# Kernel tuning notes

Hardware: AMD Instinct MI355X
Metric: run time of the kernel (lower is better)

The kernel has to match this reference:

```python
import jax, jax.numpy as jnp
import numpy as np

BLOCK = 32      # block_size
KB = 128        # K // BLOCK (mask rows)
NB = 128        # N // BLOCK (mask cols)
DENSITY = 0.1


def _make_mask_indices():
    rng = np.random.RandomState(0)
    mask = rng.rand(KB, NB) < DENSITY
    # guarantee no fully-empty output column (kernel writes zeros there anyway,
    # segment_sum also yields zeros, so this is only to keep stats sane)
    ii, jj = np.nonzero(mask)   # row-major order == torch.nonzero(mask)
    return ii.astype(np.int32), jj.astype(np.int32)


def setup_inputs() -> dict:
    key = jax.random.key(0)
    k1, k2 = jax.random.split(key)
    ii, jj = _make_mask_indices()
    nnz = ii.shape[0]
    M = 4096
    K = KB * BLOCK
    x = jax.random.normal(k1, (M, K), dtype=jnp.float32)
    # block-sparse weight: one [BLOCK, BLOCK] tile per nonzero mask entry,
    # stored in row-major nonzero order (matches torch.nonzero ordering)
    w = jax.random.normal(k2, (nnz, BLOCK, BLOCK), dtype=jnp.float32) * 0.02
    return {"x": x, "w": w, "idx_i": jnp.asarray(ii), "idx_j": jnp.asarray(jj)}


def reference(x, w, idx_i, idx_j):
    # y[:, j*B:(j+1)*B] += x[:, i*B:(i+1)*B] @ w[blk] for each nonzero block (i, j)
    M, K = x.shape
    nnz, B, _ = w.shape
    xb = x.reshape(M, K // B, B)[:, idx_i, :]                 # [M, nnz, B] gather
    partial = jnp.einsum('mnk,nkj->nmj', xb, w)               # [nnz, M, B]
    yb = jax.ops.segment_sum(partial, idx_j, num_segments=NB)  # [NB, M, B] scatter-add
    return yb.transpose(1, 0, 2).reshape(M, NB * B)           # [M, N]
```

## Files before the change

kernel.cpp:

```cpp
#include <hip/hip_runtime.h>
#include <hip/hip_bf16.h>

typedef __bf16 bf16x8 __attribute__((ext_vector_type(8)));
typedef __bf16 bf16x4 __attribute__((ext_vector_type(4)));
typedef float f32x4 __attribute__((ext_vector_type(4)));

#define KDIM 4096
#define NDIM 4096
#define NBJ  128
#define KB   128

#define NB      7
#define BLK_LDS 2560

__global__ __launch_bounds__(256) void k_prep(
    const float* __restrict__ x, const float* __restrict__ w,
    const int* __restrict__ idx_i, const int* __restrict__ idx_j,
    __bf16* __restrict__ xb, __bf16* __restrict__ wT,
    int* __restrict__ colptr, int* __restrict__ colinfo,
    int nnz, int M, int nbCvt) {
    __shared__ char smem[2176];
    int b = blockIdx.x, t = threadIdx.x;

    if (b < nbCvt) {
        int i  = b & (KB - 1);
        int m0 = (b >> 7) * 64;
        int q  = t & 3, r = t >> 2;
        const float* xp = x + (size_t)(m0 + r) * KDIM + i * 32 + q * 8;
        float4 u = ((const float4*)xp)[0];
        float4 v = ((const float4*)xp)[1];
        bf16x8 o;
        o[0]=(__bf16)u.x; o[1]=(__bf16)u.y; o[2]=(__bf16)u.z; o[3]=(__bf16)u.w;
        o[4]=(__bf16)v.x; o[5]=(__bf16)v.y; o[6]=(__bf16)v.z; o[7]=(__bf16)v.w;
        *(bf16x8*)(xb + ((size_t)i * M + m0 + r) * 32 + q * 8) = o;
    } else if (b < nbCvt + nnz) {
        auto tile = (__bf16(*)[33])smem;
        int n = b - nbCvt;
        float4 v = ((const float4*)(w + (size_t)n * 1024))[t];
        int e = t * 4, k = e >> 5, c = e & 31;
        tile[k][c + 0] = (__bf16)v.x; tile[k][c + 1] = (__bf16)v.y;
        tile[k][c + 2] = (__bf16)v.z; tile[k][c + 3] = (__bf16)v.w;
        __syncthreads();
        int f = t * 4, cc = f >> 5, kk = f & 31;
        bf16x4 o;
        o[0] = tile[kk + 0][cc]; o[1] = tile[kk + 1][cc];
        o[2] = tile[kk + 2][cc]; o[3] = tile[kk + 3][cc];
        ((bf16x4*)(wT + (size_t)n * 1024))[t] = o;
    } else {
        int* cnt = (int*)smem;
        int* cur = cnt + NBJ;
        if (t < NBJ) cnt[t] = 0;
        __syncthreads();
        for (int n = t; n < nnz; n += 256) atomicAdd(&cnt[idx_j[n]], 1);
        __syncthreads();
        int mycount = (t < NBJ) ? cnt[t] : 0;
        for (int off = 1; off < NBJ; off <<= 1) {
            int add = (t < NBJ && t >= off) ? cnt[t - off] : 0;
            __syncthreads();
            if (t < NBJ) cnt[t] += add;
            __syncthreads();
        }
        if (t < NBJ) {
            colptr[t + 1] = cnt[t];
            cur[t] = cnt[t] - mycount;
            if (t == 0) colptr[0] = 0;
        }
        __syncthreads();
        for (int n = t; n < nnz; n += 256) {
            int j = idx_j[n];
            int pos = atomicAdd(&cur[j], 1);
            colinfo[pos] = (idx_i[n] << 16) | n;
        }
    }
}

struct AFrag { bf16x8 a0, a1; };

#define MFMA4(A, B0, B1)                                                       \
    acc[0][0] = __builtin_amdgcn_mfma_f32_16x16x32_bf16(A.a0, B0, acc[0][0], 0, 0, 0); \
    acc[0][1] = __builtin_amdgcn_mfma_f32_16x16x32_bf16(A.a0, B1, acc[0][1], 0, 0, 0); \
    acc[1][0] = __builtin_amdgcn_mfma_f32_16x16x32_bf16(A.a1, B0, acc[1][0], 0, 0, 0); \
    acc[1][1] = __builtin_amdgcn_mfma_f32_16x16x32_bf16(A.a1, B1, acc[1][1], 0, 0, 0);

__global__ __launch_bounds__(256, 8) void k_bsmm(
    const __bf16* __restrict__ xb, const __bf16* __restrict__ wT,
    const int* __restrict__ colptr, const int* __restrict__ colinfo,
    float* __restrict__ y, int M) {
    __shared__ int nfo[NB];
    __shared__ __attribute__((aligned(16))) char wbuf[NB * BLK_LDS];

    int RCH = M >> 7;
    int l = blockIdx.x;
    int rc, j;
    if ((RCH & 7) == 0) {
        int rps = RCH >> 3;
        int s = l & 7, u = l >> 3;
        rc = s * rps + (u >> 7);
        j  = u & (NBJ - 1);
    } else {
        rc = l % RCH; j = l / RCH;
    }
    int t = threadIdx.x;
    int lane = t & 63, wave = t >> 6;
    int quad = lane >> 4, l16 = lane & 15;
    int wrow = rc * 128 + wave * 32;

    int beg = colptr[j], end = colptr[j + 1];

    f32x4 acc[2][2] = {};

    size_t strideA = (size_t)M * 32;
    const __bf16* xbase = xb + (size_t)(wrow + l16) * 32 + quad * 8;
    const char*   wread = wbuf + l16 * 80 + quad * 16;

    for (int bb = beg; bb < end; bb += NB) {
        int cb = end - bb; if (cb > NB) cb = NB;
        if (bb > beg) __syncthreads();
        if (t < cb) nfo[t] = colinfo[bb + t];
        __syncthreads();

        for (int c = t; c < cb * 128; c += 256) {
            int b = c >> 7, w16 = c & 127;
            int n = nfo[b] & 0xFFFF;
            bf16x8 v = *(const bf16x8*)(wT + (size_t)n * 1024 + w16 * 8);
            *(bf16x8*)(wbuf + b * BLK_LDS + (w16 >> 2) * 80 + (w16 & 3) * 16) = v;
        }
        __syncthreads();

        auto fa = [&](int p) {
            int pp = p < cb ? p : cb - 1;
            int ib = nfo[pp] >> 16;
            AFrag f;
            const __bf16* xp = xbase + (size_t)ib * strideA;
            f.a0 = *(const bf16x8*)(xp);
            f.a1 = *(const bf16x8*)(xp + 16 * 32);
            return f;
        };
        AFrag A0 = fa(0);
        AFrag A1 = fa(1);
        for (int p = 0; p < cb; ++p) {
            const char* wp = wread + p * BLK_LDS;
            bf16x8 b0 = *(const bf16x8*)(wp);
            bf16x8 b1 = *(const bf16x8*)(wp + 16 * 80);
            MFMA4(A0, b0, b1);
            A0 = A1; A1 = fa(p + 2);
        }
    }

    #pragma unroll
    for (int r = 0; r < 2; ++r)
        #pragma unroll
        for (int ch = 0; ch < 2; ++ch)
            #pragma unroll
            for (int reg = 0; reg < 4; ++reg) {
                int row = wrow + r * 16 + quad * 4 + reg;
                int col = j * 32 + ch * 16 + l16;
                y[(size_t)row * NDIM + col] = acc[r][ch][reg];
            }
}

__global__ __launch_bounds__(256) void k_bsmm_nows(
    const float* __restrict__ x, const float* __restrict__ w,
    const int* __restrict__ idx_i, const int* __restrict__ idx_j,
    float* __restrict__ y, int nnz) {
    __shared__ int list[256];
    __shared__ int listn;
    __shared__ __bf16 tw[32][40];
    int j = blockIdx.y;
    int tid = threadIdx.x;
    int lane = tid & 63, wave = tid >> 6;
    int quad = lane >> 4, l16 = lane & 15;
    int wrow = blockIdx.x * 256 + wave * 64;

    if (tid == 0) listn = 0;
    __syncthreads();
    for (int n = tid; n < nnz; n += 256)
        if (idx_j[n] == j) { int p = atomicAdd(&listn, 1); list[p & 255] = n; }
    __syncthreads();
    int cnt = listn;

    f32x4 acc[4][2] = {};
    for (int p = 0; p < cnt; ++p) {
        int n = list[p];
        int ib = idx_i[n];
        {
            float4 v = ((const float4*)(w + (size_t)n * 1024))[tid];
            int e = tid * 4, k = e >> 5, c = e & 31;
            tw[c + 0][k] = (__bf16)v.x; tw[c + 1][k] = (__bf16)v.y;
            tw[c + 2][k] = (__bf16)v.z; tw[c + 3][k] = (__bf16)v.w;
        }
        __syncthreads();
        bf16x8 a[4];
        #pragma unroll
        for (int r = 0; r < 4; ++r) {
            const float* xp = x + (size_t)(wrow + r * 16 + l16) * KDIM + ib * 32 + quad * 8;
            float4 u = *(const float4*)(xp);
            float4 v = *(const float4*)(xp + 4);
            a[r][0] = (__bf16)u.x; a[r][1] = (__bf16)u.y; a[r][2] = (__bf16)u.z; a[r][3] = (__bf16)u.w;
            a[r][4] = (__bf16)v.x; a[r][5] = (__bf16)v.y; a[r][6] = (__bf16)v.z; a[r][7] = (__bf16)v.w;
        }
        bf16x8 b0 = *(const bf16x8*)&tw[l16][quad * 8];
        bf16x8 b1 = *(const bf16x8*)&tw[l16 + 16][quad * 8];
        #pragma unroll
        for (int r = 0; r < 4; ++r) {
            acc[r][0] = __builtin_amdgcn_mfma_f32_16x16x32_bf16(a[r], b0, acc[r][0], 0, 0, 0);
            acc[r][1] = __builtin_amdgcn_mfma_f32_16x16x32_bf16(a[r], b1, acc[r][1], 0, 0, 0);
        }
        __syncthreads();
    }

    #pragma unroll
    for (int r = 0; r < 4; ++r)
        #pragma unroll
        for (int ch = 0; ch < 2; ++ch)
            #pragma unroll
            for (int reg = 0; reg < 4; ++reg) {
                int row = wrow + r * 16 + quad * 4 + reg;
                int col = j * 32 + ch * 16 + l16;
                y[(size_t)row * NDIM + col] = acc[r][ch][reg];
            }
}

extern "C" void kernel_launch(void* const* d_in, const int* in_sizes, int n_in,
                              void* d_out, int out_size, void* d_ws, size_t ws_size,
                              hipStream_t stream) {
    const float* x     = (const float*)d_in[0];
    const float* w     = (const float*)d_in[1];
    const int*   idx_i = (const int*)d_in[2];
    const int*   idx_j = (const int*)d_in[3];
    float*       y     = (float*)d_out;

    int nnz = in_sizes[2];
    int M   = in_sizes[0] / KDIM;

    size_t xb_bytes = (size_t)M * KDIM * 2;
    size_t wt_bytes = (size_t)nnz * 1024 * 2;
    size_t need = xb_bytes + wt_bytes + (size_t)(NBJ + 2 + nnz) * 4;

    if (ws_size >= need && (M & 255) == 0 && nnz < 65536) {
        __bf16* xb      = (__bf16*)d_ws;
        __bf16* wT      = (__bf16*)((char*)d_ws + xb_bytes);
        int*    colptr  = (int*)((char*)d_ws + xb_bytes + wt_bytes);
        int*    colinfo = colptr + NBJ + 1;
        int nbCvt = KB * (M / 64);
        k_prep<<<nbCvt + nnz + 1, 256, 0, stream>>>(x, w, idx_i, idx_j,
                                                    xb, wT, colptr, colinfo,
                                                    nnz, M, nbCvt);
        k_bsmm<<<(M / 128) * NBJ, 256, 0, stream>>>(xb, wT, colptr, colinfo, y, M);
    } else {
        k_bsmm_nows<<<dim3(M / 256, NBJ), 256, 0, stream>>>(x, w, idx_i, idx_j, y, nnz);
    }
}
```

Baseline: 167.2 us.

## Prefetch next weight-block chunk into registers while computing current chunk

Loads all column metadata into shared memory once, then for each chunk of up to NB weight blocks issues global loads for the next chunk into registers before running the MFMA loop on the current chunk, writing them to LDS afterward. This is meant to hide weight-load latency behind compute instead of serializing load, sync and compute. It adds 4 bf16x8 registers per thread, which may pressure occupancy under launch_bounds(256,8), and keeps the old path for columns with more than 64 blocks.

```diff
diff --git a/kernel.cpp b/kernel.cpp
--- a/kernel.cpp
+++ b/kernel.cpp
@@ -86,7 +86,7 @@
     const __bf16* __restrict__ xb, const __bf16* __restrict__ wT,
     const int* __restrict__ colptr, const int* __restrict__ colinfo,
     float* __restrict__ y, int M) {
-    __shared__ int nfo[NB];
+    __shared__ int nfo[64];
     __shared__ __attribute__((aligned(16))) char wbuf[NB * BLK_LDS];
 
     int RCH = M >> 7;
@@ -106,6 +106,7 @@
     int wrow = rc * 128 + wave * 32;
 
     int beg = colptr[j], end = colptr[j + 1];
+    int cnt = end - beg;
 
     f32x4 acc[2][2] = {};
 
@@ -113,37 +114,101 @@
     const __bf16* xbase = xb + (size_t)(wrow + l16) * 32 + quad * 8;
     const char*   wread = wbuf + l16 * 80 + quad * 16;
 
-    for (int bb = beg; bb < end; bb += NB) {
-        int cb = end - bb; if (cb > NB) cb = NB;
-        if (bb > beg) __syncthreads();
-        if (t < cb) nfo[t] = colinfo[bb + t];
-        __syncthreads();
-
-        for (int c = t; c < cb * 128; c += 256) {
-            int b = c >> 7, w16 = c & 127;
-            int n = nfo[b] & 0xFFFF;
-            bf16x8 v = *(const bf16x8*)(wT + (size_t)n * 1024 + w16 * 8);
-            *(bf16x8*)(wbuf + b * BLK_LDS + (w16 >> 2) * 80 + (w16 & 3) * 16) = v;
-        }
-        __syncthreads();
-
-        auto fa = [&](int p) {
-            int pp = p < cb ? p : cb - 1;
-            int ib = nfo[pp] >> 16;
-            AFrag f;
-            const __bf16* xp = xbase + (size_t)ib * strideA;
-            f.a0 = *(const bf16x8*)(xp);
-            f.a1 = *(const bf16x8*)(xp + 16 * 32);
-            return f;
+    if (cnt > 0 && cnt <= 64) {
+        if (t < cnt) nfo[t] = colinfo[beg + t];
+        __syncthreads();
+
+        bf16x8 S[4];
+        auto sload = [&](int b0, int cbl) {
+            #pragma unroll
+            for (int i = 0; i < 4; ++i) {
+                int c = t + i * 256;
+                if (c < cbl * 128) {
+                    int b = c >> 7, w16 = c & 127;
+                    int n = nfo[b0 + b] & 0xFFFF;
+                    S[i] = *(const bf16x8*)(wT + (size_t)n * 1024 + w16 * 8);
+                }
+            }
         };
-        AFrag A0 = fa(0);
-        AFrag A1 = fa(1);
-        for (int p = 0; p < cb; ++p) {
-            const char* wp = wread + p * BLK_LDS;
-            bf16x8 b0 = *(const bf16x8*)(wp);
-            bf16x8 b1 = *(const bf16x8*)(wp + 16 * 80);
-            MFMA4(A0, b0, b1);
-            A0 = A1; A1 = fa(p + 2);
+        auto swrite = [&](int cbl) {
+            #pragma unroll
+            for (int i = 0; i < 4; ++i) {
+                int c = t + i * 256;
+                if (c < cbl * 128) {
+                    int b = c >> 7, w16 = c & 127;
+                    *(bf16x8*)(wbuf + b * BLK_LDS + (w16 >> 2) * 80 + (w16 & 3) * 16) = S[i];
+                }
+            }
+        };
+
+        int bb = 0;
+        int cb = cnt < NB ? cnt : NB;
+        sload(0, cb);
+        swrite(cb);
+        __syncthreads();
+
+        for (;;) {
+            int bbn = bb + cb;
+            int cbn = cnt - bbn; if (cbn > NB) cbn = NB;
+
+            auto fa = [&](int p) {
+                int pp = p < cb ? p : cb - 1;
+                int ib = nfo[bb + pp] >> 16;
+                AFrag f;
+                const __bf16* xp = xbase + (size_t)ib * strideA;
+                f.a0 = *(const bf16x8*)(xp);
+                f.a1 = *(const bf16x8*)(xp + 16 * 32);
+                return f;
+            };
+            AFrag A0 = fa(0);
+            AFrag A1 = fa(1);
+            if (cbn > 0) sload(bbn, cbn);
+
+            for (int p = 0; p < cb; ++p) {
+                const char* wp = wread + p * BLK_LDS;
+                bf16x8 b0 = *(const bf16x8*)(wp);
+                bf16x8 b1 = *(const bf16x8*)(wp + 16 * 80);
+                MFMA4(A0, b0, b1);
+                A0 = A1; A1 = fa(p + 2);
+            }
+
+            if (cbn <= 0) break;
+            __syncthreads();
+            swrite(cbn);
+            __syncthreads();
+            bb = bbn; cb = cbn;
+        }
+    } else if (cnt > 64) {
+        for (int bb = beg; bb < end; bb += NB) {
+            int cb = end - bb; if (cb > NB) cb = NB;
+            if (bb > beg) __syncthreads();
+            if (t < cb) nfo[t] = colinfo[bb + t];
+            __syncthreads();
+            for (int c = t; c < cb * 128; c += 256) {
+                int b = c >> 7, w16 = c & 127;
+                int n = nfo[b] & 0xFFFF;
+                bf16x8 v = *(const bf16x8*)(wT + (size_t)n * 1024 + w16 * 8);
+                *(bf16x8*)(wbuf + b * BLK_LDS + (w16 >> 2) * 80 + (w16 & 3) * 16) = v;
+            }
+            __syncthreads();
+            auto fa = [&](int p) {
+                int pp = p < cb ? p : cb - 1;
+                int ib = nfo[pp] >> 16;
+                AFrag f;
+                const __bf16* xp = xbase + (size_t)ib * strideA;
+                f.a0 = *(const bf16x8*)(xp);
+                f.a1 = *(const bf16x8*)(xp + 16 * 32);
+                return f;
+            };
+            AFrag A0 = fa(0);
+            AFrag A1 = fa(1);
+            for (int p = 0; p < cb; ++p) {
+                const char* wp = wread + p * BLK_LDS;
+                bf16x8 b0 = *(const bf16x8*)(wp);
+                bf16x8 b1 = *(const bf16x8*)(wp + 16 * 80);
+                MFMA4(A0, b0, b1);
+                A0 = A1; A1 = fa(p + 2);
+            }
         }
     }
 
```

Result: slower. 193.1 us (+15.5%).
